# Kernel tuning notes

Measured on AMD Instinct MI355X. Metric: run time of the kernel, lower is better.

Reference implementation:

```python
import jax, jax.numpy as jnp
import numpy as np

OUT_H, OUT_W = 7, 7
SPATIAL_SCALE = 0.25
SAMPLE_NUM = 2  # sampling grid per bin is SAMPLE_NUM x SAMPLE_NUM


def setup_inputs() -> dict:
    key = jax.random.key(0)
    k1, k2, k3, k4, k5, k6 = jax.random.split(key, 6)
    B, C, H, W = 2, 256, 200, 200
    features = jax.random.normal(k1, (B, C, H, W), dtype=jnp.float32)
    N = 512
    # rois: (batch_idx, cx, cy, w, h, theta) in image coords (image = 800x800)
    bidx = jax.random.randint(k2, (N,), 0, B).astype(jnp.float32)
    cx = jax.random.uniform(k3, (N,), jnp.float32, 100.0, 700.0)
    cy = jax.random.uniform(k4, (N,), jnp.float32, 100.0, 700.0)
    wh = jax.random.uniform(k5, (N, 2), jnp.float32, 32.0, 256.0)
    ang = jax.random.uniform(k6, (N,), jnp.float32, -np.pi / 2, np.pi / 2)
    rois = jnp.concatenate(
        [bidx[:, None], cx[:, None], cy[:, None], wh, ang[:, None]], axis=1
    )
    return {"features": features, "rois": rois}


def _rroi_align(features, rois):
    B, C, H, W = features.shape
    N = rois.shape[0]
    batch_idx = rois[:, 0].astype(jnp.int32)
    cx = rois[:, 1] * SPATIAL_SCALE
    cy = rois[:, 2] * SPATIAL_SCALE
    rw = jnp.maximum(rois[:, 3] * SPATIAL_SCALE, 1.0)
    rh = jnp.maximum(rois[:, 4] * SPATIAL_SCALE, 1.0)
    theta = rois[:, 5]

    bin_h = rh / OUT_H
    bin_w = rw / OUT_W

    ph = jnp.arange(OUT_H, dtype=jnp.float32)
    pw = jnp.arange(OUT_W, dtype=jnp.float32)
    frac = (jnp.arange(SAMPLE_NUM, dtype=jnp.float32) + 0.5) / SAMPLE_NUM

    # local (un-rotated) offsets from roi center
    # yy: [N, OUT_H, S], xx: [N, OUT_W, S]
    yy = -rh[:, None, None] / 2 + (ph[None, :, None] + frac[None, None, :]) * bin_h[:, None, None]
    xx = -rw[:, None, None] / 2 + (pw[None, :, None] + frac[None, None, :]) * bin_w[:, None, None]

    cosT = jnp.cos(theta)[:, None, None, None, None]
    sinT = jnp.sin(theta)[:, None, None, None, None]
    yy_ = yy[:, :, None, :, None]  # [N, OH, 1, Sy, 1]
    xx_ = xx[:, None, :, None, :]  # [N, 1, OW, 1, Sx]
    # rotate into feature-map coords (RRPN/mmcv convention)
    x = xx_ * cosT + yy_ * sinT + cx[:, None, None, None, None]  # [N,OH,OW,Sy,Sx]
    y = yy_ * cosT - xx_ * sinT + cy[:, None, None, None, None]

    valid = (y > -1.0) & (y < H) & (x > -1.0) & (x < W)
    y = jnp.clip(y, 0.0, H - 1)
    x = jnp.clip(x, 0.0, W - 1)

    y0 = jnp.clip(jnp.floor(y), 0, H - 2).astype(jnp.int32)
    x0 = jnp.clip(jnp.floor(x), 0, W - 2).astype(jnp.int32)
    y1 = y0 + 1
    x1 = x0 + 1
    ly = y - y0.astype(jnp.float32)
    lx = x - x0.astype(jnp.float32)
    hy = 1.0 - ly
    hx = 1.0 - lx

    b = batch_idx[:, None, None, None, None]  # [N,1,1,1,1]

    def gather(yi, xi):
        # advanced indices (b, yi, xi) separated by the channel slice ->
        # result shape [N, OH, OW, Sy, Sx, C]
        return features[b, :, yi, xi]

    val = (
        (hy * hx)[..., None] * gather(y0, x0)
        + (hy * lx)[..., None] * gather(y0, x1)
        + (ly * hx)[..., None] * gather(y1, x0)
        + (ly * lx)[..., None] * gather(y1, x1)
    )
    val = jnp.where(valid[..., None], val, 0.0)
    # average over the SAMPLE_NUM x SAMPLE_NUM grid per bin
    out = val.mean(axis=(3, 4))  # [N, OH, OW, C]
    return jnp.transpose(out, (0, 3, 1, 2))  # [N, C, OH, OW]


def reference(features, rois):
    return _rroi_align(features, rois)
```

## Files before the change

### kernel.cpp

```cpp
#include <hip/hip_runtime.h>

constexpr int B_ = 2, C_ = 256, H_ = 200, W_ = 200;
constexpr int HW_ = H_ * W_;
constexpr int N_ROIS = 512;
constexpr int OUT_H_ = 7, OUT_W_ = 7;
constexpr float SPATIAL_SCALE_ = 0.25f;
constexpr int NBIN = OUT_H_ * OUT_W_;
constexpr int OUT_PER_ROI = C_ * NBIN;

__global__ __launch_bounds__(256) void transpose_cl_kernel(
    const float* __restrict__ in, float* __restrict__ out) {
    __shared__ float tile[64][68];
    const int b  = blockIdx.z;
    const int p0 = blockIdx.x * 64;
    const int c0 = blockIdx.y * 64;
    const int tid = threadIdx.x;
    const int hi = tid >> 4;
    const int lo = tid & 15;

    const float* src = in  + (size_t)b * C_ * HW_;
    float*       dst = out + (size_t)b * HW_ * C_;

#pragma unroll
    for (int j = 0; j < 4; ++j) {
        const int cr = hi + j * 16;
        const int pm = lo * 4;
        const float4 v = *(const float4*)(src + (size_t)(c0 + cr) * HW_ + p0 + pm);
        tile[pm + 0][cr] = v.x;
        tile[pm + 1][cr] = v.y;
        tile[pm + 2][cr] = v.z;
        tile[pm + 3][cr] = v.w;
    }
    __syncthreads();
#pragma unroll
    for (int j = 0; j < 4; ++j) {
        const int pr = hi + j * 16;
        const int cm = lo * 4;
        const float4 r = *(const float4*)&tile[pr][cm];
        *(float4*)(dst + (size_t)(p0 + pr) * C_ + c0 + cm) = r;
    }
}

__global__ __launch_bounds__(256) void rroi_gather_kernel(
    const float* __restrict__ feat_cl,
    const float* __restrict__ rois,
    float* __restrict__ out) {
    __shared__ float  s_out[OUT_PER_ROI];
    __shared__ int    s_off[196];
    __shared__ float4 s_w[196];

    const int n   = blockIdx.x;
    const int tid = threadIdx.x;

    const float* roi = rois + (size_t)n * 6;
    const int   b     = (int)roi[0];
    const float cx    = roi[1] * SPATIAL_SCALE_;
    const float cy    = roi[2] * SPATIAL_SCALE_;
    const float rw    = fmaxf(roi[3] * SPATIAL_SCALE_, 1.0f);
    const float rh    = fmaxf(roi[4] * SPATIAL_SCALE_, 1.0f);
    const float theta = roi[5];
    const float bin_h = rh / (float)OUT_H_;
    const float bin_w = rw / (float)OUT_W_;

    if (tid < 196) {
        const float cosT = cosf(theta);
        const float sinT = sinf(theta);
        const int bin = tid >> 2;
        const int s   = tid & 3;
        const int ph  = bin / OUT_W_;
        const int pw  = bin - ph * OUT_W_;
        const int s1  = s >> 1;
        const int s2  = s & 1;

        const float yy = -rh * 0.5f + ((float)ph + ((float)s1 + 0.5f) * 0.5f) * bin_h;
        const float xx = -rw * 0.5f + ((float)pw + ((float)s2 + 0.5f) * 0.5f) * bin_w;

        float x = xx * cosT + yy * sinT + cx;
        float y = yy * cosT - xx * sinT + cy;

        const bool valid = (y > -1.0f) && (y < (float)H_) &&
                           (x > -1.0f) && (x < (float)W_);

        y = fminf(fmaxf(y, 0.0f), (float)(H_ - 1));
        x = fminf(fmaxf(x, 0.0f), (float)(W_ - 1));
        int y0 = (int)floorf(y);  if (y0 > H_ - 2) y0 = H_ - 2;
        int x0 = (int)floorf(x);  if (x0 > W_ - 2) x0 = W_ - 2;

        const float ly = y - (float)y0;
        const float lx = x - (float)x0;
        const float hy = 1.0f - ly;
        const float hx = 1.0f - lx;
        const float m  = valid ? 0.25f : 0.0f;

        s_w[tid]   = make_float4(hy * hx * m, hy * lx * m, ly * hx * m, ly * lx * m);
        s_off[tid] = (y0 * W_ + x0) * C_;
    }
    __syncthreads();

    const int wave = tid >> 6;
    const int lane = tid & 63;
    const float* base = feat_cl + (size_t)b * HW_ * C_ + 4 * lane;

    for (int bin = wave; bin < NBIN; bin += 4) {
        float4 acc = make_float4(0.f, 0.f, 0.f, 0.f);
#pragma unroll
        for (int s = 0; s < 4; ++s) {
            const int j = bin * 4 + s;
            const int off = s_off[j];
            const float4 w = s_w[j];
            const float* p = base + off;
            const float4 f00 = *(const float4*)p;
            const float4 f01 = *(const float4*)(p + C_);
            const float4 f10 = *(const float4*)(p + W_ * C_);
            const float4 f11 = *(const float4*)(p + W_ * C_ + C_);
            acc.x += w.x * f00.x + w.y * f01.x + w.z * f10.x + w.w * f11.x;
            acc.y += w.x * f00.y + w.y * f01.y + w.z * f10.y + w.w * f11.y;
            acc.z += w.x * f00.z + w.y * f01.z + w.z * f10.z + w.w * f11.z;
            acc.w += w.x * f00.w + w.y * f01.w + w.z * f10.w + w.w * f11.w;
        }
        const int c = 4 * lane;
        s_out[(c + 0) * NBIN + bin] = acc.x;
        s_out[(c + 1) * NBIN + bin] = acc.y;
        s_out[(c + 2) * NBIN + bin] = acc.z;
        s_out[(c + 3) * NBIN + bin] = acc.w;
    }
    __syncthreads();

    float4* o = (float4*)(out + (size_t)n * OUT_PER_ROI);
    const float4* l = (const float4*)s_out;
#pragma unroll
    for (int k = 0; k < 12; ++k) {
        o[tid + 256 * k] = l[tid + 256 * k];
    }
    if (tid < 64) o[3072 + tid] = l[3072 + tid];
}

__global__ __launch_bounds__(64) void rroi_fallback_kernel(
    const float* __restrict__ feat,
    const float* __restrict__ rois,
    float* __restrict__ out) {
    const int blk = blockIdx.x;
    const int n   = blk / NBIN;
    const int bin = blk % NBIN;
    const int ph  = bin / OUT_W_;
    const int pw  = bin % OUT_W_;

    const float* roi = rois + (size_t)n * 6;
    const int   b     = (int)roi[0];
    const float cx    = roi[1] * SPATIAL_SCALE_;
    const float cy    = roi[2] * SPATIAL_SCALE_;
    const float rw    = fmaxf(roi[3] * SPATIAL_SCALE_, 1.0f);
    const float rh    = fmaxf(roi[4] * SPATIAL_SCALE_, 1.0f);
    const float theta = roi[5];
    const float bin_h = rh / (float)OUT_H_;
    const float bin_w = rw / (float)OUT_W_;
    const float cosT  = cosf(theta);
    const float sinT  = sinf(theta);
    const int t = threadIdx.x;
    float acc[4] = {0.f, 0.f, 0.f, 0.f};

#pragma unroll
    for (int s1 = 0; s1 < 2; ++s1) {
        const float yy = -rh * 0.5f + ((float)ph + ((float)s1 + 0.5f) * 0.5f) * bin_h;
#pragma unroll
        for (int s2 = 0; s2 < 2; ++s2) {
            const float xx = -rw * 0.5f + ((float)pw + ((float)s2 + 0.5f) * 0.5f) * bin_w;
            float x = xx * cosT + yy * sinT + cx;
            float y = yy * cosT - xx * sinT + cy;
            const bool valid = (y > -1.0f) && (y < (float)H_) &&
                               (x > -1.0f) && (x < (float)W_);
            if (!valid) continue;
            y = fminf(fmaxf(y, 0.0f), (float)(H_ - 1));
            x = fminf(fmaxf(x, 0.0f), (float)(W_ - 1));
            int y0 = (int)floorf(y);  if (y0 > H_ - 2) y0 = H_ - 2;
            int x0 = (int)floorf(x);  if (x0 > W_ - 2) x0 = W_ - 2;
            const float ly = y - (float)y0, lx = x - (float)x0;
            const float hy = 1.0f - ly, hx = 1.0f - lx;
            const float w00 = hy * hx, w01 = hy * lx, w10 = ly * hx, w11 = ly * lx;
            const int off0 = y0 * W_ + x0;
#pragma unroll
            for (int i = 0; i < 4; ++i) {
                const float* base = feat + ((size_t)b * C_ + 4 * t + i) * HW_;
                acc[i] += w00 * base[off0] + w01 * base[off0 + 1] +
                          w10 * base[off0 + W_] + w11 * base[off0 + W_ + 1];
            }
        }
    }
#pragma unroll
    for (int i = 0; i < 4; ++i) {
        out[((size_t)n * C_ + (4 * t + i)) * NBIN + bin] = acc[i] * 0.25f;
    }
}

extern "C" void kernel_launch(void* const* d_in, const int* in_sizes, int n_in,
                              void* d_out, int out_size, void* d_ws, size_t ws_size,
                              hipStream_t stream) {
    const float* features = (const float*)d_in[0];
    const float* rois     = (const float*)d_in[1];
    float* out = (float*)d_out;

    const size_t need = (size_t)B_ * C_ * HW_ * sizeof(float);
    if (ws_size >= need) {
        float* feat_cl = (float*)d_ws;
        dim3 tg(HW_ / 64, C_ / 64, B_);
        transpose_cl_kernel<<<tg, 256, 0, stream>>>(features, feat_cl);
        rroi_gather_kernel<<<N_ROIS, 256, 0, stream>>>(feat_cl, rois, out);
    } else {
        rroi_fallback_kernel<<<N_ROIS * NBIN, 64, 0, stream>>>(features, rois, out);
    }
}
```

Before: 180.6 us.

## Sort ROIs spatially, widen gather blocks, and use nontemporal loads/stores

Adds a single-block rank-sort kernel that orders ROIs by batch and coarse center position. Gather blocks are assigned ROIs from this permutation, interleaved across eight groups, so that spatially nearby ROIs likely run on the same XCD and reuse L2-cached feature rows. The gather kernel now uses 512 threads, with 8 waves over the bins. The transpose loads and output stores are marked nontemporal to reduce cache pollution. This adds an extra kernel launch and a small workspace, and the 512-thread blocks with large shared memory may lower occupancy.

```diff
diff --git a/kernel.cpp b/kernel.cpp
--- a/kernel.cpp
+++ b/kernel.cpp
@@ -7,6 +7,27 @@
 constexpr float SPATIAL_SCALE_ = 0.25f;
 constexpr int NBIN = OUT_H_ * OUT_W_;
 constexpr int OUT_PER_ROI = C_ * NBIN;
+
+using f32x4 = __attribute__((ext_vector_type(4))) float;
+
+__global__ __launch_bounds__(512) void roi_sort_kernel(
+    const float* __restrict__ rois, int* __restrict__ perm) {
+    __shared__ unsigned s_key[N_ROIS];
+    const int i = threadIdx.x;
+    const float* roi = rois + (size_t)i * 6;
+    const int b  = (int)roi[0];
+    const int ix = (int)(roi[1] * SPATIAL_SCALE_) & 255;
+    const int iy = (int)(roi[2] * SPATIAL_SCALE_) & 255;
+    const unsigned key = ((unsigned)b << 16) | ((unsigned)iy << 8) | (unsigned)ix;
+    s_key[i] = key;
+    __syncthreads();
+    int rank = 0;
+    for (int j = 0; j < N_ROIS; ++j) {
+        const unsigned kj = s_key[j];
+        rank += (kj < key) || (kj == key && j < i);
+    }
+    perm[rank] = i;
+}
 
 __global__ __launch_bounds__(256) void transpose_cl_kernel(
     const float* __restrict__ in, float* __restrict__ out) {
@@ -25,7 +46,8 @@
     for (int j = 0; j < 4; ++j) {
         const int cr = hi + j * 16;
         const int pm = lo * 4;
-        const float4 v = *(const float4*)(src + (size_t)(c0 + cr) * HW_ + p0 + pm);
+        const f32x4 v = __builtin_nontemporal_load(
+            (const f32x4*)(src + (size_t)(c0 + cr) * HW_ + p0 + pm));
         tile[pm + 0][cr] = v.x;
         tile[pm + 1][cr] = v.y;
         tile[pm + 2][cr] = v.z;
@@ -41,15 +63,18 @@
     }
 }
 
-__global__ __launch_bounds__(256) void rroi_gather_kernel(
+__global__ __launch_bounds__(512) void rroi_gather_kernel(
     const float* __restrict__ feat_cl,
     const float* __restrict__ rois,
+    const int* __restrict__ perm,
     float* __restrict__ out) {
     __shared__ float  s_out[OUT_PER_ROI];
     __shared__ int    s_off[196];
     __shared__ float4 s_w[196];
 
-    const int n   = blockIdx.x;
+    const int bid = blockIdx.x;
+    const int sorted = (bid & 7) * (N_ROIS / 8) + (bid >> 3);
+    const int n = perm ? perm[sorted] : bid;
     const int tid = threadIdx.x;
 
     const float* roi = rois + (size_t)n * 6;
@@ -101,7 +126,7 @@
     const int lane = tid & 63;
     const float* base = feat_cl + (size_t)b * HW_ * C_ + 4 * lane;
 
-    for (int bin = wave; bin < NBIN; bin += 4) {
+    for (int bin = wave; bin < NBIN; bin += 8) {
         float4 acc = make_float4(0.f, 0.f, 0.f, 0.f);
 #pragma unroll
         for (int s = 0; s < 4; ++s) {
@@ -126,13 +151,13 @@
     }
     __syncthreads();
 
-    float4* o = (float4*)(out + (size_t)n * OUT_PER_ROI);
-    const float4* l = (const float4*)s_out;
-#pragma unroll
-    for (int k = 0; k < 12; ++k) {
-        o[tid + 256 * k] = l[tid + 256 * k];
-    }
-    if (tid < 64) o[3072 + tid] = l[3072 + tid];
+    f32x4* o = (f32x4*)(out + (size_t)n * OUT_PER_ROI);
+    const f32x4* l = (const f32x4*)s_out;
+#pragma unroll
+    for (int k = 0; k < 6; ++k) {
+        __builtin_nontemporal_store(l[tid + 512 * k], o + tid + 512 * k);
+    }
+    if (tid < 64) __builtin_nontemporal_store(l[3072 + tid], o + 3072 + tid);
 }
 
 __global__ __launch_bounds__(64) void rroi_fallback_kernel(
@@ -199,12 +224,21 @@
     const float* rois     = (const float*)d_in[1];
     float* out = (float*)d_out;
 
-    const size_t need = (size_t)B_ * C_ * HW_ * sizeof(float);
-    if (ws_size >= need) {
+    const size_t feat_bytes = (size_t)B_ * C_ * HW_ * sizeof(float);
+    const size_t perm_bytes = (size_t)N_ROIS * sizeof(int);
+
+    if (ws_size >= feat_bytes + perm_bytes) {
+        float* feat_cl = (float*)d_ws;
+        int*   perm    = (int*)((char*)d_ws + feat_bytes);
+        roi_sort_kernel<<<1, 512, 0, stream>>>(rois, perm);
+        dim3 tg(HW_ / 64, C_ / 64, B_);
+        transpose_cl_kernel<<<tg, 256, 0, stream>>>(features, feat_cl);
+        rroi_gather_kernel<<<N_ROIS, 512, 0, stream>>>(feat_cl, rois, perm, out);
+    } else if (ws_size >= feat_bytes) {
         float* feat_cl = (float*)d_ws;
         dim3 tg(HW_ / 64, C_ / 64, B_);
         transpose_cl_kernel<<<tg, 256, 0, stream>>>(features, feat_cl);
-        rroi_gather_kernel<<<N_ROIS, 256, 0, stream>>>(feat_cl, rois, out);
+        rroi_gather_kernel<<<N_ROIS, 512, 0, stream>>>(feat_cl, rois, nullptr, out);
     } else {
         rroi_fallback_kernel<<<N_ROIS * NBIN, 64, 0, stream>>>(features, rois, out);
     }
```

Result: no change. 179.1 us (-0.8%).
